# Kernel optimization log

Measured on AMD Instinct MI355X. Metric: run time of the kernel, lower is better.

## Reference

```python
import jax, jax.numpy as jnp
import numpy as np
from jax import lax

WINDOW = 7
PAD = WINDOW // 2  # 3
C1 = 0.01 ** 2
C2 = 0.03 ** 2


def _box_sum(x):
    # Equivalent to conv2d with an all-ones 7x7 kernel, padding=3 (NCHW).
    return lax.reduce_window(
        x, 0.0, lax.add,
        window_dimensions=(1, 1, WINDOW, WINDOW),
        window_strides=(1, 1, 1, 1),
        padding=((0, 0), (0, 0), (PAD, PAD), (PAD, PAD)),
    )


def setup_inputs() -> dict:
    key = jax.random.key(0)
    k1, k2 = jax.random.split(key)
    shape = (64, 1, 512, 512)
    img1 = jax.random.uniform(k1, shape, dtype=jnp.float32)
    img2 = jax.random.uniform(k2, shape, dtype=jnp.float32)
    return {"img1": img1, "img2": img2}


def reference(img1, img2):
    mu1 = _box_sum(img1)
    mu2 = _box_sum(img2)
    sigma1_sq = _box_sum(img1 * img1) - mu1 * mu1
    sigma2_sq = _box_sum(img2 * img2) - mu2 * mu2
    sigma12 = _box_sum(img1 * img2) - mu1 * mu2
    ssim_map = ((2.0 * mu1 * mu2 + C1) * (2.0 * sigma12 + C2)) / (
        (mu1 * mu1 + mu2 * mu2 + C1) * (sigma1_sq + sigma2_sq + C2)
    )
    return 1.0 - jnp.mean(ssim_map)
```

## Files before the change

### kernel.cpp

```cpp
#include <hip/hip_runtime.h>


constexpr int IMG = 512;
constexpr int TW = 128;
constexpr int TH = 64;
constexpr int LROWS = TH + 6;
constexpr int PITCH = 136;
constexpr int F4_PER_ROW = PITCH / 4;
constexpr int NSTAGE = LROWS * F4_PER_ROW;
constexpr float C1 = 1.0e-4f;
constexpr float C2 = 9.0e-4f;
constexpr double INV_N = 1.0 / (64.0 * 512.0 * 512.0);

__global__ __launch_bounds__(256, 2)
void ssim_fused(const float* __restrict__ img1, const float* __restrict__ img2,
                double* __restrict__ partial) {
    __shared__ float sa[LROWS][PITCH];
    __shared__ float sb[LROWS][PITCH];
    __shared__ float wpart[4];

    const int tid = threadIdx.x;
    const int tx0 = blockIdx.x * TW;
    const int ty0 = blockIdx.y * TH;
    const size_t ib = (size_t)blockIdx.z * (IMG * IMG);
    const float* b1 = img1 + ib;
    const float* b2 = img2 + ib;

    for (int idx = tid; idx < NSTAGE; idx += 256) {
        int r = idx / F4_PER_ROW;
        int c4 = idx - r * F4_PER_ROW;
        int gy = ty0 - 3 + r;
        int gx = tx0 - 4 + 4 * c4;
        float4 va = make_float4(0.f, 0.f, 0.f, 0.f);
        float4 vb = make_float4(0.f, 0.f, 0.f, 0.f);
        if ((unsigned)gy < (unsigned)IMG && (unsigned)gx < (unsigned)IMG) {
            int g = gy * IMG + gx;
            va = *(const float4*)(b1 + g);
            vb = *(const float4*)(b2 + g);
        }
        *(float4*)&sa[r][4 * c4] = va;
        *(float4*)&sb[r][4 * c4] = vb;
    }
    __syncthreads();

    const int l = tid & 63;
    const int seg = tid >> 6;
    const int y0 = seg * 16;
    const int cb = 2 * l;

    float rA0[8], rA1[8], rB0[8], rB1[8], rAA0[8], rAA1[8],
          rBB0[8], rBB1[8], rAB0[8], rAB1[8];
    float SA0 = 0, SA1 = 0, SB0 = 0, SB1 = 0, SAA0 = 0, SAA1 = 0,
          SBB0 = 0, SBB1 = 0, SAB0 = 0, SAB1 = 0;
    float acc = 0.f;

    auto hrow = [&](int rr, int k) {
        const float2* pa = (const float2*)&sa[rr][cb];
        const float2* pb = (const float2*)&sb[rr][cb];
        float2 a0 = pa[0], a1 = pa[1], a2 = pa[2], a3 = pa[3], a4 = pa[4];
        float2 b0 = pb[0], b1v = pb[1], b2v = pb[2], b3 = pb[3], b4 = pb[4];
        float va1 = a0.y, va2 = a1.x, va3 = a1.y, va4 = a2.x,
              va5 = a2.y, va6 = a3.x, va7 = a3.y, va8 = a4.x;
        float vb1 = b0.y, vb2 = b1v.x, vb3 = b1v.y, vb4 = b2v.x,
              vb5 = b2v.y, vb6 = b3.x, vb7 = b3.y, vb8 = b4.x;

        float sA = ((va1 + va2) + (va3 + va4)) + ((va5 + va6) + va7);
        rA0[k] = sA;
        rA1[k] = (sA - va1) + va8;

        float sB = ((vb1 + vb2) + (vb3 + vb4)) + ((vb5 + vb6) + vb7);
        rB0[k] = sB;
        rB1[k] = (sB - vb1) + vb8;

        float sAA = fmaf(va7, va7, fmaf(va6, va6, fmaf(va5, va5,
                    fmaf(va4, va4, fmaf(va3, va3, fmaf(va2, va2, va1 * va1))))));
        rAA0[k] = sAA;
        rAA1[k] = fmaf(va8, va8, sAA - va1 * va1);

        float sBB = fmaf(vb7, vb7, fmaf(vb6, vb6, fmaf(vb5, vb5,
                    fmaf(vb4, vb4, fmaf(vb3, vb3, fmaf(vb2, vb2, vb1 * vb1))))));
        rBB0[k] = sBB;
        rBB1[k] = fmaf(vb8, vb8, sBB - vb1 * vb1);

        float sAB = fmaf(va7, vb7, fmaf(va6, vb6, fmaf(va5, vb5,
                    fmaf(va4, vb4, fmaf(va3, vb3, fmaf(va2, vb2, va1 * vb1))))));
        rAB0[k] = sAB;
        rAB1[k] = fmaf(va8, vb8, sAB - va1 * vb1);
    };

#pragma unroll
    for (int k = 0; k < 6; ++k) {
        hrow(y0 + k, k);
        SA0 += rA0[k]; SA1 += rA1[k]; SB0 += rB0[k]; SB1 += rB1[k];
        SAA0 += rAA0[k]; SAA1 += rAA1[k]; SBB0 += rBB0[k]; SBB1 += rBB1[k];
        SAB0 += rAB0[k]; SAB1 += rAB1[k];
    }

#pragma unroll
    for (int t = 0; t < 16; ++t) {
        const int kn = (t + 6) & 7;
        const int ko = t & 7;
        hrow(y0 + t + 6, kn);
        SA0 += rA0[kn]; SA1 += rA1[kn]; SB0 += rB0[kn]; SB1 += rB1[kn];
        SAA0 += rAA0[kn]; SAA1 += rAA1[kn]; SBB0 += rBB0[kn]; SBB1 += rBB1[kn];
        SAB0 += rAB0[kn]; SAB1 += rAB1[kn];

        {
            float m12 = SA0 * SB0, m11 = SA0 * SA0, m22 = SB0 * SB0;
            float num = fmaf(2.f, m12, C1) * fmaf(2.f, SAB0 - m12, C2);
            float den = (m11 + m22 + C1) * ((SAA0 - m11) + (SBB0 - m22) + C2);
            acc += num / den;
        }
        {
            float m12 = SA1 * SB1, m11 = SA1 * SA1, m22 = SB1 * SB1;
            float num = fmaf(2.f, m12, C1) * fmaf(2.f, SAB1 - m12, C2);
            float den = (m11 + m22 + C1) * ((SAA1 - m11) + (SBB1 - m22) + C2);
            acc += num / den;
        }

        SA0 -= rA0[ko]; SA1 -= rA1[ko]; SB0 -= rB0[ko]; SB1 -= rB1[ko];
        SAA0 -= rAA0[ko]; SAA1 -= rAA1[ko]; SBB0 -= rBB0[ko]; SBB1 -= rBB1[ko];
        SAB0 -= rAB0[ko]; SAB1 -= rAB1[ko];
    }

#pragma unroll
    for (int off = 32; off > 0; off >>= 1)
        acc += __shfl_xor(acc, off);
    if (l == 0) wpart[seg] = acc;
    __syncthreads();
    if (tid == 0)
        atomicAdd(partial, (double)((wpart[0] + wpart[1]) + (wpart[2] + wpart[3])));
}

__global__ void ssim_finalize(const double* __restrict__ partial,
                              float* __restrict__ out) {
    out[0] = (float)(1.0 - partial[0] * INV_N);
}

extern "C" void kernel_launch(void* const* d_in, const int* in_sizes, int n_in,
                              void* d_out, int out_size, void* d_ws, size_t ws_size,
                              hipStream_t stream) {
    const float* img1 = (const float*)d_in[0];
    const float* img2 = (const float*)d_in[1];
    float* out = (float*)d_out;
    double* partial = (double*)d_ws;

    hipMemsetAsync(partial, 0, sizeof(double), stream);

    dim3 grid(IMG / TW, IMG / TH, 64);
    ssim_fused<<<grid, 256, 0, stream>>>(img1, img2, partial);
    ssim_finalize<<<1, 1, 0, stream>>>(partial, out);
}
```

Baseline: 176.8 us.

## Replace LDS tile staging with direct global row loads over full-width bands

Removes the shared-memory staging of 70x136 tiles and the barrier, and instead has each thread load its overlapping float2 row segments straight from global memory (relying on the caches) for 16-row bands spanning the full 512-pixel width. Occupancy hint is raised to 4 blocks per SM, and the exact division is replaced with a hardware reciprocal plus fma. The trade-off is redundant global/L1 loads (5 float2 per image per row per thread) and more vertical halo re-reads because bands are short, along with slightly lower precision in the division.

```diff
diff --git a/kernel.cpp b/kernel.cpp
--- a/kernel.cpp
+++ b/kernel.cpp
@@ -2,51 +2,32 @@
 
 
 constexpr int IMG = 512;
-constexpr int TW = 128;
-constexpr int TH = 64;
-constexpr int LROWS = TH + 6;
-constexpr int PITCH = 136;
-constexpr int F4_PER_ROW = PITCH / 4;
-constexpr int NSTAGE = LROWS * F4_PER_ROW;
+constexpr int BAND = 16;
 constexpr float C1 = 1.0e-4f;
 constexpr float C2 = 9.0e-4f;
 constexpr double INV_N = 1.0 / (64.0 * 512.0 * 512.0);
 
-__global__ __launch_bounds__(256, 2)
+__global__ __launch_bounds__(256, 4)
 void ssim_fused(const float* __restrict__ img1, const float* __restrict__ img2,
                 double* __restrict__ partial) {
-    __shared__ float sa[LROWS][PITCH];
-    __shared__ float sb[LROWS][PITCH];
     __shared__ float wpart[4];
 
     const int tid = threadIdx.x;
-    const int tx0 = blockIdx.x * TW;
-    const int ty0 = blockIdx.y * TH;
-    const size_t ib = (size_t)blockIdx.z * (IMG * IMG);
+    const int y0 = blockIdx.x * BAND;
+    const size_t ib = (size_t)blockIdx.y * (IMG * IMG);
     const float* b1 = img1 + ib;
     const float* b2 = img2 + ib;
 
-    for (int idx = tid; idx < NSTAGE; idx += 256) {
-        int r = idx / F4_PER_ROW;
-        int c4 = idx - r * F4_PER_ROW;
-        int gy = ty0 - 3 + r;
-        int gx = tx0 - 4 + 4 * c4;
-        float4 va = make_float4(0.f, 0.f, 0.f, 0.f);
-        float4 vb = make_float4(0.f, 0.f, 0.f, 0.f);
-        if ((unsigned)gy < (unsigned)IMG && (unsigned)gx < (unsigned)IMG) {
-            int g = gy * IMG + gx;
-            va = *(const float4*)(b1 + g);
-            vb = *(const float4*)(b2 + g);
-        }
-        *(float4*)&sa[r][4 * c4] = va;
-        *(float4*)&sb[r][4 * c4] = vb;
-    }
-    __syncthreads();
-
-    const int l = tid & 63;
-    const int seg = tid >> 6;
-    const int y0 = seg * 16;
-    const int cb = 2 * l;
+    const int xb = 2 * tid;
+    const int xo0 = max(xb - 4, 0);
+    const int xo1 = max(xb - 2, 0);
+    const int xo2 = xb;
+    const int xo3 = min(xb + 2, IMG - 2);
+    const int xo4 = min(xb + 4, IMG - 2);
+    const bool p0 = (xb - 4) >= 0;
+    const bool p1 = (xb - 2) >= 0;
+    const bool p3 = (xb + 2) < IMG;
+    const bool p4 = (xb + 4) < IMG;
 
     float rA0[8], rA1[8], rB0[8], rB1[8], rAA0[8], rAA1[8],
           rBB0[8], rBB1[8], rAB0[8], rAB1[8];
@@ -54,15 +35,32 @@
           SBB0 = 0, SBB1 = 0, SAB0 = 0, SAB1 = 0;
     float acc = 0.f;
 
-    auto hrow = [&](int rr, int k) {
-        const float2* pa = (const float2*)&sa[rr][cb];
-        const float2* pb = (const float2*)&sb[rr][cb];
-        float2 a0 = pa[0], a1 = pa[1], a2 = pa[2], a3 = pa[3], a4 = pa[4];
-        float2 b0 = pb[0], b1v = pb[1], b2v = pb[2], b3 = pb[3], b4 = pb[4];
+    auto hrow = [&](int row, int k) {
+        float2 zz = make_float2(0.f, 0.f);
+        float2 a0 = zz, a1 = zz, a2 = zz, a3 = zz, a4 = zz;
+        float2 c0 = zz, c1v = zz, c2v = zz, c3 = zz, c4 = zz;
+        if ((unsigned)row < (unsigned)IMG) {
+            const float* r1 = b1 + row * IMG;
+            const float* r2 = b2 + row * IMG;
+            a0 = *(const float2*)(r1 + xo0);
+            a1 = *(const float2*)(r1 + xo1);
+            a2 = *(const float2*)(r1 + xo2);
+            a3 = *(const float2*)(r1 + xo3);
+            a4 = *(const float2*)(r1 + xo4);
+            c0 = *(const float2*)(r2 + xo0);
+            c1v = *(const float2*)(r2 + xo1);
+            c2v = *(const float2*)(r2 + xo2);
+            c3 = *(const float2*)(r2 + xo3);
+            c4 = *(const float2*)(r2 + xo4);
+            a0 = p0 ? a0 : zz;  c0 = p0 ? c0 : zz;
+            a1 = p1 ? a1 : zz;  c1v = p1 ? c1v : zz;
+            a3 = p3 ? a3 : zz;  c3 = p3 ? c3 : zz;
+            a4 = p4 ? a4 : zz;  c4 = p4 ? c4 : zz;
+        }
         float va1 = a0.y, va2 = a1.x, va3 = a1.y, va4 = a2.x,
               va5 = a2.y, va6 = a3.x, va7 = a3.y, va8 = a4.x;
-        float vb1 = b0.y, vb2 = b1v.x, vb3 = b1v.y, vb4 = b2v.x,
-              vb5 = b2v.y, vb6 = b3.x, vb7 = b3.y, vb8 = b4.x;
+        float vb1 = c0.y, vb2 = c1v.x, vb3 = c1v.y, vb4 = c2v.x,
+              vb5 = c2v.y, vb6 = c3.x, vb7 = c3.y, vb8 = c4.x;
 
         float sA = ((va1 + va2) + (va3 + va4)) + ((va5 + va6) + va7);
         rA0[k] = sA;
@@ -90,17 +88,17 @@
 
 #pragma unroll
     for (int k = 0; k < 6; ++k) {
-        hrow(y0 + k, k);
+        hrow(y0 - 3 + k, k);
         SA0 += rA0[k]; SA1 += rA1[k]; SB0 += rB0[k]; SB1 += rB1[k];
         SAA0 += rAA0[k]; SAA1 += rAA1[k]; SBB0 += rBB0[k]; SBB1 += rBB1[k];
         SAB0 += rAB0[k]; SAB1 += rAB1[k];
     }
 
 #pragma unroll
-    for (int t = 0; t < 16; ++t) {
+    for (int t = 0; t < BAND; ++t) {
         const int kn = (t + 6) & 7;
         const int ko = t & 7;
-        hrow(y0 + t + 6, kn);
+        hrow(y0 + t + 3, kn);
         SA0 += rA0[kn]; SA1 += rA1[kn]; SB0 += rB0[kn]; SB1 += rB1[kn];
         SAA0 += rAA0[kn]; SAA1 += rAA1[kn]; SBB0 += rBB0[kn]; SBB1 += rBB1[kn];
         SAB0 += rAB0[kn]; SAB1 += rAB1[kn];
@@ -109,13 +107,13 @@
             float m12 = SA0 * SB0, m11 = SA0 * SA0, m22 = SB0 * SB0;
             float num = fmaf(2.f, m12, C1) * fmaf(2.f, SAB0 - m12, C2);
             float den = (m11 + m22 + C1) * ((SAA0 - m11) + (SBB0 - m22) + C2);
-            acc += num / den;
+            acc = fmaf(num, __builtin_amdgcn_rcpf(den), acc);
         }
         {
             float m12 = SA1 * SB1, m11 = SA1 * SA1, m22 = SB1 * SB1;
             float num = fmaf(2.f, m12, C1) * fmaf(2.f, SAB1 - m12, C2);
             float den = (m11 + m22 + C1) * ((SAA1 - m11) + (SBB1 - m22) + C2);
-            acc += num / den;
+            acc = fmaf(num, __builtin_amdgcn_rcpf(den), acc);
         }
 
         SA0 -= rA0[ko]; SA1 -= rA1[ko]; SB0 -= rB0[ko]; SB1 -= rB1[ko];
@@ -126,7 +124,7 @@
 #pragma unroll
     for (int off = 32; off > 0; off >>= 1)
         acc += __shfl_xor(acc, off);
-    if (l == 0) wpart[seg] = acc;
+    if ((tid & 63) == 0) wpart[tid >> 6] = acc;
     __syncthreads();
     if (tid == 0)
         atomicAdd(partial, (double)((wpart[0] + wpart[1]) + (wpart[2] + wpart[3])));
@@ -147,7 +145,7 @@
 
     hipMemsetAsync(partial, 0, sizeof(double), stream);
 
-    dim3 grid(IMG / TW, IMG / TH, 64);
+    dim3 grid(IMG / BAND, 64);
     ssim_fused<<<grid, 256, 0, stream>>>(img1, img2, partial);
     ssim_finalize<<<1, 1, 0, stream>>>(partial, out);
 }
```

New measurement: 383.7 us. +117.1%, slower.
